# Performance work log

Measured on AMD Instinct MI355X. Metric: run time of the kernel, lower is better.

Reference implementation:

```python
import jax, jax.numpy as jnp
import numpy as np

B, M, N, T = 8192, 4, 8, 512  # groups, measurements, states, timesteps


def setup_inputs() -> dict:
    key = jax.random.key(0)
    k0, k1, k2, k3, k4, k5 = jax.random.split(key, 6)
    x = jax.random.normal(k0, (B, M, T), dtype=jnp.float32)
    # stable transition matrix (spectral radius < 1)
    F = (0.9 * jnp.eye(N) + 0.05 * jax.random.normal(k1, (N, N)) / np.sqrt(N)).astype(jnp.float32)
    H = (jax.random.normal(k2, (M, N)) / np.sqrt(N)).astype(jnp.float32)
    qa = jax.random.normal(k3, (N, N))
    Q = (0.05 * (qa @ qa.T) / N + 0.01 * jnp.eye(N)).astype(jnp.float32)
    ra = jax.random.normal(k4, (M, M))
    R = (0.1 * (ra @ ra.T) / M + 0.05 * jnp.eye(M)).astype(jnp.float32)
    initial_std_dev = (1.0 + jax.random.uniform(k5, (N,))).astype(jnp.float32)
    return {"x": x, "F": F, "H": H, "Q": Q, "R": R, "initial_std_dev": initial_std_dev}


def _kf_forward(x, F, H, Q, R, initial_std_dev):
    b, m, t = x.shape
    n = F.shape[0]
    dt = x.dtype
    # default_initializer: mean = 0 (len(initial_state)==num_states path with zeros),
    # cov = quad_form_diag(std, eye) = diag(std^2)
    mean0 = jnp.zeros((b, n, 1), dt)
    cov0 = jnp.broadcast_to(jnp.diag(initial_std_dev ** 2).astype(dt), (b, n, n))
    I_n = jnp.eye(n, dtype=dt)

    def step(carry, obs_t):  # obs_t: [b, m]
        mu, P = carry  # [b,n,1], [b,n,n]
        # --- predict ---
        mu = jnp.einsum('ij,bjk->bik', F, mu)
        P = jnp.einsum('ij,bjk,lk->bil', F, P, F) + Q
        out = jnp.einsum('mj,bjo->bmo', H, mu)[..., 0]  # [b, m]
        # --- update (no NaNs in obs -> update all slices) ---
        resid = obs_t[..., None] - out[..., None]  # [b,m,1]
        HP = jnp.einsum('mj,bjk->bmk', H, P)  # [b,m,n]
        S = jnp.einsum('bmj,nj->bmn', HP, H) + R  # [b,m,m]
        Sinv = jnp.linalg.inv(S)
        PHt = jnp.swapaxes(HP, 1, 2)  # P symmetric => P H^T = (H P)^T, [b,n,m]
        K = jnp.einsum('bnm,bmo->bno', PHt, Sinv)  # [b,n,m]
        mu_new = mu + jnp.einsum('bnm,bmo->bno', K, resid)
        # Joseph-stabilized covariance update
        ImKH = I_n - jnp.einsum('bnm,mj->bnj', K, H)  # [b,n,n]
        P_new = (jnp.einsum('bij,bjk,blk->bil', ImKH, P, ImKH)
                 + jnp.einsum('bim,mo,bko->bik', K, R, K))
        return (mu_new, P_new), out

    xs = jnp.moveaxis(x, 2, 0)  # [t, b, m]
    _, outs = jax.lax.scan(step, (mean0, cov0), xs)
    return jnp.moveaxis(outs, 0, 2)  # [b, m, t]


def reference(x, F, H, Q, R, initial_std_dev):
    return _kf_forward(x, F, H, Q, R, initial_std_dev)
```

## Files before the change

### kernel.cpp

```cpp
#include <hip/hip_runtime.h>


#define B_BATCH 8192
#define M_MEAS 4
#define N_ST 8
#define T_STEPS 512
#define CHUNK 16
#define NCHUNK (T_STEPS / CHUNK)

__device__ __forceinline__ void kf_producer(
    const float* __restrict__ Fp, const float* __restrict__ Hp,
    const float* __restrict__ Qp, const float* __restrict__ Rp,
    const float* __restrict__ stdp, float* __restrict__ Kws, int* flag)
{
    const int lane = threadIdx.x;
    const int i = lane >> 3, j = lane & 7;
    __shared__ float Pm[64], T1m[64], Vm[32], PPm[64], Am[64], Bm[64], Km[32];

    float Fi[8], Fj[8], Hm[4][8], HFm[4][8], HFr[8], QHi[4];
    float R2[4][4], Rr[4][4];
#pragma unroll
    for (int k = 0; k < 8; ++k) { Fi[k] = Fp[8 * i + k]; Fj[k] = Fp[8 * j + k]; }
#pragma unroll
    for (int m = 0; m < 4; ++m)
#pragma unroll
        for (int k = 0; k < 8; ++k) Hm[m][k] = Hp[8 * m + k];
#pragma unroll
    for (int m = 0; m < 4; ++m)
#pragma unroll
        for (int c = 0; c < 8; ++c) {
            float a = 0.f;
#pragma unroll
            for (int k = 0; k < 8; ++k) a += Hm[m][k] * Fp[8 * k + c];
            HFm[m][c] = a;
        }
#pragma unroll
    for (int c = 0; c < 8; ++c) {
        float a = 0.f;
#pragma unroll
        for (int k = 0; k < 8; ++k) a += Hp[8 * (i & 3) + k] * Fp[8 * k + c];
        HFr[c] = a;
    }
    const float Qij = Qp[lane];
#pragma unroll
    for (int m = 0; m < 4; ++m) {
        float a = 0.f;
#pragma unroll
        for (int k = 0; k < 8; ++k) a += Qp[8 * i + k] * Hm[m][k];
        QHi[m] = a;
    }
    {
        float HQ[4][8];
#pragma unroll
        for (int m = 0; m < 4; ++m)
#pragma unroll
            for (int c = 0; c < 8; ++c) {
                float a = 0.f;
#pragma unroll
                for (int l = 0; l < 8; ++l) a += Hm[m][l] * Qp[8 * l + c];
                HQ[m][c] = a;
            }
#pragma unroll
        for (int m = 0; m < 4; ++m)
#pragma unroll
            for (int n = 0; n < 4; ++n) {
                float a = Rp[4 * m + n];
#pragma unroll
                for (int k = 0; k < 8; ++k) a += HQ[m][k] * Hm[n][k];
                R2[m][n] = a;
                Rr[m][n] = Rp[4 * m + n];
            }
    }
    float pold;
    { float s0 = stdp[i]; pold = (i == j) ? s0 * s0 : 0.f; Pm[lane] = pold; }
    __syncthreads();

    int convcnt = 0;
    for (int t = 0; t < T_STEPS; ++t) {
        float4 pa = *(const float4*)&Pm[8 * j];
        float4 pb = *(const float4*)&Pm[8 * j + 4];
        float Pc[8] = {pa.x, pa.y, pa.z, pa.w, pb.x, pb.y, pb.z, pb.w};
        float t1 = 0.f, uo = 0.f;
#pragma unroll
        for (int k = 0; k < 8; ++k) { t1 += Fi[k] * Pc[k]; uo += HFr[k] * Pc[k]; }
        T1m[lane] = t1;
        if (i < 4) Vm[8 * i + j] = uo;
        __syncthreads();

        float4 ta = *(const float4*)&T1m[8 * i];
        float4 tb = *(const float4*)&T1m[8 * i + 4];
        float T1r[8] = {ta.x, ta.y, ta.z, ta.w, tb.x, tb.y, tb.z, tb.w};
        float pp = Qij;
#pragma unroll
        for (int k = 0; k < 8; ++k) pp += T1r[k] * Fj[k];
        float PPH[4];
#pragma unroll
        for (int m = 0; m < 4; ++m) {
            float a = QHi[m];
#pragma unroll
            for (int k = 0; k < 8; ++k) a += T1r[k] * HFm[m][k];
            PPH[m] = a;
        }
        PPm[lane] = pp;

        float Vr[4][8];
#pragma unroll
        for (int m = 0; m < 4; ++m) {
            float4 va = *(const float4*)&Vm[8 * m];
            float4 vb = *(const float4*)&Vm[8 * m + 4];
            Vr[m][0] = va.x; Vr[m][1] = va.y; Vr[m][2] = va.z; Vr[m][3] = va.w;
            Vr[m][4] = vb.x; Vr[m][5] = vb.y; Vr[m][6] = vb.z; Vr[m][7] = vb.w;
        }
        float S[4][4];
#pragma unroll
        for (int m = 0; m < 4; ++m)
#pragma unroll
            for (int n = m; n < 4; ++n) {
                float a = R2[m][n];
#pragma unroll
                for (int k = 0; k < 8; ++k) a += Vr[m][k] * HFm[n][k];
                S[m][n] = a; S[n][m] = a;
            }
        float SI[16];
        {
            const float A0 = S[0][0], A1 = S[0][1], A2 = S[0][2], A3 = S[0][3];
            const float A4 = S[1][0], A5 = S[1][1], A6 = S[1][2], A7 = S[1][3];
            const float A8 = S[2][0], A9 = S[2][1], A10 = S[2][2], A11 = S[2][3];
            const float A12 = S[3][0], A13 = S[3][1], A14 = S[3][2], A15 = S[3][3];
            float b00 = A0 * A5 - A1 * A4, b01 = A0 * A6 - A2 * A4;
            float b02 = A0 * A7 - A3 * A4, b03 = A1 * A6 - A2 * A5;
            float b04 = A1 * A7 - A3 * A5, b05 = A2 * A7 - A3 * A6;
            float b06 = A8 * A13 - A9 * A12, b07 = A8 * A14 - A10 * A12;
            float b08 = A8 * A15 - A11 * A12, b09 = A9 * A14 - A10 * A13;
            float b10 = A9 * A15 - A11 * A13, b11 = A10 * A15 - A11 * A14;
            float det = b00 * b11 - b01 * b10 + b02 * b09 + b03 * b08 -
                        b04 * b07 + b05 * b06;
            float rd = 1.0f / det;
            SI[0]  = ( A5 * b11 - A6 * b10 + A7 * b09) * rd;
            SI[1]  = (-A1 * b11 + A2 * b10 - A3 * b09) * rd;
            SI[2]  = ( A13 * b05 - A14 * b04 + A15 * b03) * rd;
            SI[3]  = (-A9 * b05 + A10 * b04 - A11 * b03) * rd;
            SI[4]  = (-A4 * b11 + A6 * b08 - A7 * b07) * rd;
            SI[5]  = ( A0 * b11 - A2 * b08 + A3 * b07) * rd;
            SI[6]  = (-A12 * b05 + A14 * b02 - A15 * b01) * rd;
            SI[7]  = ( A8 * b05 - A10 * b02 + A11 * b01) * rd;
            SI[8]  = ( A4 * b10 - A5 * b08 + A7 * b06) * rd;
            SI[9]  = (-A0 * b10 + A1 * b08 - A3 * b06) * rd;
            SI[10] = ( A12 * b04 - A13 * b02 + A15 * b00) * rd;
            SI[11] = (-A8 * b04 + A9 * b02 - A11 * b00) * rd;
            SI[12] = (-A4 * b09 + A5 * b07 - A6 * b06) * rd;
            SI[13] = ( A0 * b09 - A1 * b07 + A2 * b06) * rd;
            SI[14] = (-A12 * b03 + A13 * b01 - A14 * b00) * rd;
            SI[15] = ( A8 * b03 - A9 * b01 + A10 * b00) * rd;
        }
        float Kl[4];
#pragma unroll
        for (int m = 0; m < 4; ++m) {
            float a = 0.f;
#pragma unroll
            for (int p = 0; p < 4; ++p) a += PPH[p] * SI[4 * p + m];
            Kl[m] = a;
        }
        float Ar[8];
#pragma unroll
        for (int c = 0; c < 8; ++c) {
            float a = (i == c) ? 1.f : 0.f;
#pragma unroll
            for (int m = 0; m < 4; ++m) a -= Kl[m] * Hm[m][c];
            Ar[c] = a;
        }
        float Ei[4];
#pragma unroll
        for (int o = 0; o < 4; ++o) {
            float a = 0.f;
#pragma unroll
            for (int m = 0; m < 4; ++m) a += Kl[m] * Rr[m][o];
            Ei[o] = a;
        }
        const float aij = (j == 0) ? Ar[0] : (j == 1) ? Ar[1]
                        : (j == 2) ? Ar[2] : (j == 3) ? Ar[3]
                        : (j == 4) ? Ar[4] : (j == 5) ? Ar[5]
                        : (j == 6) ? Ar[6] : Ar[7];
        Am[lane] = aij;
        const float kj4 = (j == 0) ? Kl[0] : (j == 1) ? Kl[1]
                        : (j == 2) ? Kl[2] : Kl[3];
        if (j < 4) {
            Km[4 * i + j] = kj4;
            Kws[t * 32 + i * 4 + j] = kj4;
        }
        __syncthreads();

        float4 qa = *(const float4*)&PPm[8 * j];
        float4 qb = *(const float4*)&PPm[8 * j + 4];
        float PPc[8] = {qa.x, qa.y, qa.z, qa.w, qb.x, qb.y, qb.z, qb.w};
        float bv = 0.f;
#pragma unroll
        for (int k = 0; k < 8; ++k) bv += Ar[k] * PPc[k];
        Bm[lane] = bv;
        float4 aja = *(const float4*)&Am[8 * j];
        float4 ajb = *(const float4*)&Am[8 * j + 4];
        float Arj[8] = {aja.x, aja.y, aja.z, aja.w, ajb.x, ajb.y, ajb.z, ajb.w};
        float4 kjv = *(const float4*)&Km[4 * j];
        float Kj[4] = {kjv.x, kjv.y, kjv.z, kjv.w};
        __syncthreads();

        float4 ba = *(const float4*)&Bm[8 * i];
        float4 bb = *(const float4*)&Bm[8 * i + 4];
        float Br[8] = {ba.x, ba.y, ba.z, ba.w, bb.x, bb.y, bb.z, bb.w};
        float acc = 0.f;
#pragma unroll
        for (int k = 0; k < 8; ++k) acc += Br[k] * Arj[k];
#pragma unroll
        for (int o = 0; o < 4; ++o) acc += Ei[o] * Kj[o];
        Pm[lane] = acc;

        const float dp = fabsf(acc - pold);
        pold = acc;
        convcnt = __all(dp <= 1.5e-6f) ? convcnt + 1 : 0;
        if (convcnt >= 2 && t >= 31 && t < T_STEPS - 1) {
            if (j < 4) {
                for (int tt = t + 1; tt < T_STEPS; ++tt)
                    Kws[tt * 32 + i * 4 + j] = kj4;
            }
            if (flag != nullptr && lane == 0) {
                __hip_atomic_store(flag + 1, t, __ATOMIC_RELAXED,
                                   __HIP_MEMORY_SCOPE_AGENT);
                __threadfence();
                __hip_atomic_store(flag, NCHUNK, __ATOMIC_RELEASE,
                                   __HIP_MEMORY_SCOPE_AGENT);
            }
            break;
        }

        if (flag != nullptr && ((t & (CHUNK - 1)) == (CHUNK - 1))) {
            if (lane == 0) {
                __threadfence();
                __hip_atomic_store(flag, (t + 1) / CHUNK, __ATOMIC_RELEASE,
                                   __HIP_MEMORY_SCOPE_AGENT);
            }
        }
        __syncthreads();
    }
}

__device__ __forceinline__ void kf_consumer(
    const float* __restrict__ xp, const float* __restrict__ Fp,
    const float* __restrict__ Hp, const float* __restrict__ Kws,
    float* __restrict__ outp, int bblk, int* flag)
{
    const int b = bblk * 64 + threadIdx.x;

    float Fv[N_ST][N_ST];
#pragma unroll
    for (int n = 0; n < N_ST; ++n)
#pragma unroll
        for (int k = 0; k < N_ST; ++k) Fv[n][k] = Fp[8 * n + k];

    float G[M_MEAS][N_ST];
#pragma unroll
    for (int m = 0; m < M_MEAS; ++m) {
#pragma unroll
        for (int n = 0; n < N_ST; ++n) {
            float acc = 0.f;
#pragma unroll
            for (int k = 0; k < N_ST; ++k) acc += Hp[8 * m + k] * Fv[k][n];
            G[m][n] = acc;
        }
    }

    float mu[N_ST];
#pragma unroll
    for (int n = 0; n < N_ST; ++n) mu[n] = 0.f;

    const float* xb = xp + (size_t)b * (M_MEAS * T_STEPS);
    float* ob = outp + (size_t)b * (M_MEAS * T_STEPS);

    int lastseen = 0, tcf = 0;
    int g = 0;
    for (; g < 32; ++g) {
        if (flag != nullptr) {
            const int need = g + 1;
            if (lastseen < need) {
                while ((lastseen = __hip_atomic_load(
                            flag, __ATOMIC_RELAXED,
                            __HIP_MEMORY_SCOPE_AGENT)) < need)
                    __builtin_amdgcn_s_sleep(16);
                __builtin_amdgcn_fence(__ATOMIC_ACQUIRE, "agent");
            }
            if (tcf == 0)
                tcf = __hip_atomic_load(flag + 1, __ATOMIC_RELAXED,
                                        __HIP_MEMORY_SCOPE_AGENT);
            if (tcf > 0 && g * 16 >= tcf) break;
        }

        float ob16[M_MEAS][16];
#pragma unroll
        for (int u = 0; u < 4; ++u) {
            const int t4 = g * 4 + u;
            float4 xq[M_MEAS];
#pragma unroll
            for (int m = 0; m < M_MEAS; ++m)
                xq[m] = *(const float4*)(xb + m * T_STEPS + t4 * 4);

#pragma unroll
            for (int s = 0; s < 4; ++s) {
                const int t = t4 * 4 + s;
                const float4* kq = (const float4*)(Kws + t * 32);
                float4 kv[N_ST];
#pragma unroll
                for (int n = 0; n < N_ST; ++n) kv[n] = kq[n];

                float resid[M_MEAS];
#pragma unroll
                for (int m = 0; m < M_MEAS; ++m) {
                    float acc = 0.f;
#pragma unroll
                    for (int n = 0; n < N_ST; ++n) acc += G[m][n] * mu[n];
                    ob16[m][u * 4 + s] = acc;
                    const float xv = (s == 0) ? xq[m].x
                                   : (s == 1) ? xq[m].y
                                   : (s == 2) ? xq[m].z : xq[m].w;
                    resid[m] = xv - acc;
                }
                float nmu[N_ST];
#pragma unroll
                for (int n = 0; n < N_ST; ++n) {
                    float acc = 0.f;
#pragma unroll
                    for (int k = 0; k < N_ST; ++k) acc += Fv[n][k] * mu[k];
                    acc += kv[n].x * resid[0] + kv[n].y * resid[1] +
                           kv[n].z * resid[2] + kv[n].w * resid[3];
                    nmu[n] = acc;
                }
#pragma unroll
                for (int n = 0; n < N_ST; ++n) mu[n] = nmu[n];
            }
        }
#pragma unroll
        for (int m = 0; m < M_MEAS; ++m)
#pragma unroll
            for (int q = 0; q < 4; ++q)
                *(float4*)(ob + m * T_STEPS + g * 16 + q * 4) =
                    make_float4(ob16[m][4 * q], ob16[m][4 * q + 1],
                                ob16[m][4 * q + 2], ob16[m][4 * q + 3]);
    }

    if (g < 32) {
        float4 kvF[N_ST];
        {
            const float4* kqF = (const float4*)(Kws + (size_t)(g * 16) * 32);
#pragma unroll
            for (int n = 0; n < N_ST; ++n) kvF[n] = kqF[n];
        }
        for (; g < 32; ++g) {
            float ob16[M_MEAS][16];
#pragma unroll
            for (int u = 0; u < 4; ++u) {
                const int t4 = g * 4 + u;
                float4 xq[M_MEAS];
#pragma unroll
                for (int m = 0; m < M_MEAS; ++m)
                    xq[m] = *(const float4*)(xb + m * T_STEPS + t4 * 4);

#pragma unroll
                for (int s = 0; s < 4; ++s) {
                    float resid[M_MEAS];
#pragma unroll
                    for (int m = 0; m < M_MEAS; ++m) {
                        float acc = 0.f;
#pragma unroll
                        for (int n = 0; n < N_ST; ++n) acc += G[m][n] * mu[n];
                        ob16[m][u * 4 + s] = acc;
                        const float xv = (s == 0) ? xq[m].x
                                       : (s == 1) ? xq[m].y
                                       : (s == 2) ? xq[m].z : xq[m].w;
                        resid[m] = xv - acc;
                    }
                    float nmu[N_ST];
#pragma unroll
                    for (int n = 0; n < N_ST; ++n) {
                        float acc = 0.f;
#pragma unroll
                        for (int k = 0; k < N_ST; ++k) acc += Fv[n][k] * mu[k];
                        acc += kvF[n].x * resid[0] + kvF[n].y * resid[1] +
                               kvF[n].z * resid[2] + kvF[n].w * resid[3];
                        nmu[n] = acc;
                    }
#pragma unroll
                    for (int n = 0; n < N_ST; ++n) mu[n] = nmu[n];
                }
            }
#pragma unroll
            for (int m = 0; m < M_MEAS; ++m)
#pragma unroll
                for (int q = 0; q < 4; ++q)
                    *(float4*)(ob + m * T_STEPS + g * 16 + q * 4) =
                        make_float4(ob16[m][4 * q], ob16[m][4 * q + 1],
                                    ob16[m][4 * q + 2], ob16[m][4 * q + 3]);
        }
    }
}

__global__ __launch_bounds__(64) void kf_kernel(
    const float* __restrict__ x, const float* __restrict__ F,
    const float* __restrict__ H, const float* __restrict__ Q,
    const float* __restrict__ R, const float* __restrict__ std0,
    float* __restrict__ Kws, int* flag, float* __restrict__ out, int role)
{
    if (role == 0) {
        if (blockIdx.x == 0) kf_producer(F, H, Q, R, std0, Kws, flag);
        else kf_consumer(x, F, H, Kws, out, (int)blockIdx.x - 1, flag);
    } else if (role == 1) {
        kf_producer(F, H, Q, R, std0, Kws, nullptr);
    } else {
        kf_consumer(x, F, H, Kws, out, (int)blockIdx.x, nullptr);
    }
}

extern "C" void kernel_launch(void* const* d_in, const int* in_sizes, int n_in,
                              void* d_out, int out_size, void* d_ws, size_t ws_size,
                              hipStream_t stream) {
    const float* x   = (const float*)d_in[0];
    const float* F   = (const float*)d_in[1];
    const float* H   = (const float*)d_in[2];
    const float* Q   = (const float*)d_in[3];
    const float* R   = (const float*)d_in[4];
    const float* s0  = (const float*)d_in[5];
    float* out = (float*)d_out;
    float* Kws = (float*)d_ws;
    const size_t KWS_BYTES = (size_t)T_STEPS * 32 * sizeof(float);

    if (ws_size >= KWS_BYTES + 256) {
        int* flag = (int*)((char*)d_ws + KWS_BYTES);
        hipMemsetAsync(flag, 0, 2 * sizeof(int), stream);
        kf_kernel<<<dim3(1 + B_BATCH / 64), dim3(64), 0, stream>>>(
            x, F, H, Q, R, s0, Kws, flag, out, 0);
    } else {
        kf_kernel<<<dim3(1), dim3(64), 0, stream>>>(
            x, F, H, Q, R, s0, Kws, (int*)nullptr, out, 1);
        kf_kernel<<<dim3(B_BATCH / 64), dim3(64), 0, stream>>>(
            x, F, H, Q, R, s0, Kws, (int*)nullptr, out, 2);
    }
}
```

Before: 355.9 us.

## Replace producer LDS exchanges with cross-lane permutes; prefetch observations in consumer tail

The single-wave producer that runs the covariance recursion no longer exchanges P, T1, V, PP, A, K and B through shared memory with barriers. It now moves values between lanes with ds_bpermute and computes S = H·PP·Hᵀ through ds_swizzle butterfly reductions, which removes every __syncthreads from the serial 512-step loop. The consumer's tail loop is flattened to one iteration per 4 steps and loads observations two iterations ahead to hide global-load latency. The flattened loop indexes ob16 with a runtime value, which may push that array into scratch memory.

```diff
diff --git a/kernel.cpp b/kernel.cpp
--- a/kernel.cpp
+++ b/kernel.cpp
@@ -7,6 +7,14 @@
 #define T_STEPS 512
 #define CHUNK 16
 #define NCHUNK (T_STEPS / CHUNK)
+
+__device__ __forceinline__ float bperm_f(int byte_addr, float v) {
+    return __int_as_float(
+        __builtin_amdgcn_ds_bpermute(byte_addr, __float_as_int(v)));
+}
+#define SWZ_ADD(p, imm)                                                     \
+    p += __int_as_float(                                                    \
+        __builtin_amdgcn_ds_swizzle(__float_as_int(p), imm))
 
 __device__ __forceinline__ void kf_producer(
     const float* __restrict__ Fp, const float* __restrict__ Hp,
@@ -15,9 +23,15 @@
 {
     const int lane = threadIdx.x;
     const int i = lane >> 3, j = lane & 7;
-    __shared__ float Pm[64], T1m[64], Vm[32], PPm[64], Am[64], Bm[64], Km[32];
-
-    float Fi[8], Fj[8], Hm[4][8], HFm[4][8], HFr[8], QHi[4];
+
+    int A1[8], A2[8];
+#pragma unroll
+    for (int k = 0; k < 8; ++k) {
+        A1[k] = (8 * j + k) * 4;
+        A2[k] = (8 * i + k) * 4;
+    }
+
+    float Fi[8], Fj[8], Hm[4][8], HFm[4][8], HFr[8], QHi[4], HFcol[4];
     float R2[4][4], Rr[4][4];
 #pragma unroll
     for (int k = 0; k < 8; ++k) { Fi[k] = Fp[8 * i + k]; Fj[k] = Fp[8 * j + k]; }
@@ -40,6 +54,18 @@
 #pragma unroll
         for (int k = 0; k < 8; ++k) a += Hp[8 * (i & 3) + k] * Fp[8 * k + c];
         HFr[c] = a;
+    }
+    {
+        float Fcol[8];
+#pragma unroll
+        for (int k = 0; k < 8; ++k) Fcol[k] = Fp[8 * k + j];
+#pragma unroll
+        for (int n = 0; n < 4; ++n) {
+            float a = 0.f;
+#pragma unroll
+            for (int k = 0; k < 8; ++k) a += Hm[n][k] * Fcol[k];
+            HFcol[n] = a;
+        }
     }
     const float Qij = Qp[lane];
 #pragma unroll
@@ -71,28 +97,29 @@
                 Rr[m][n] = Rp[4 * m + n];
             }
     }
-    float pold;
-    { float s0 = stdp[i]; pold = (i == j) ? s0 * s0 : 0.f; Pm[lane] = pold; }
-    __syncthreads();
+
+    float pv, pold;
+    { float s0 = stdp[i]; pv = (i == j) ? s0 * s0 : 0.f; pold = pv; }
 
     int convcnt = 0;
     for (int t = 0; t < T_STEPS; ++t) {
-        float4 pa = *(const float4*)&Pm[8 * j];
-        float4 pb = *(const float4*)&Pm[8 * j + 4];
-        float Pc[8] = {pa.x, pa.y, pa.z, pa.w, pb.x, pb.y, pb.z, pb.w};
+        float Pc[8];
+#pragma unroll
+        for (int k = 0; k < 8; ++k) Pc[k] = bperm_f(A1[k], pv);
         float t1 = 0.f, uo = 0.f;
 #pragma unroll
         for (int k = 0; k < 8; ++k) { t1 += Fi[k] * Pc[k]; uo += HFr[k] * Pc[k]; }
-        T1m[lane] = t1;
-        if (i < 4) Vm[8 * i + j] = uo;
-        __syncthreads();
-
-        float4 ta = *(const float4*)&T1m[8 * i];
-        float4 tb = *(const float4*)&T1m[8 * i + 4];
-        float T1r[8] = {ta.x, ta.y, ta.z, ta.w, tb.x, tb.y, tb.z, tb.w};
+
+        float T1r[8];
+#pragma unroll
+        for (int k = 0; k < 8; ++k) T1r[k] = bperm_f(A2[k], t1);
         float pp = Qij;
 #pragma unroll
         for (int k = 0; k < 8; ++k) pp += T1r[k] * Fj[k];
+        float PPc[8];
+#pragma unroll
+        for (int k = 0; k < 8; ++k) PPc[k] = bperm_f(A1[k], pp);
+
         float PPH[4];
 #pragma unroll
         for (int m = 0; m < 4; ++m) {
@@ -101,35 +128,33 @@
             for (int k = 0; k < 8; ++k) a += T1r[k] * HFm[m][k];
             PPH[m] = a;
         }
-        PPm[lane] = pp;
-
-        float Vr[4][8];
+
+        float p0 = uo * HFcol[0], p1 = uo * HFcol[1];
+        float p2 = uo * HFcol[2], p3 = uo * HFcol[3];
+        SWZ_ADD(p0, 0x041F); SWZ_ADD(p1, 0x041F);
+        SWZ_ADD(p2, 0x041F); SWZ_ADD(p3, 0x041F);
+        SWZ_ADD(p0, 0x081F); SWZ_ADD(p1, 0x081F);
+        SWZ_ADD(p2, 0x081F); SWZ_ADD(p3, 0x081F);
+        SWZ_ADD(p0, 0x101F); SWZ_ADD(p1, 0x101F);
+        SWZ_ADD(p2, 0x101F); SWZ_ADD(p3, 0x101F);
+        float S[4][4];
 #pragma unroll
         for (int m = 0; m < 4; ++m) {
-            float4 va = *(const float4*)&Vm[8 * m];
-            float4 vb = *(const float4*)&Vm[8 * m + 4];
-            Vr[m][0] = va.x; Vr[m][1] = va.y; Vr[m][2] = va.z; Vr[m][3] = va.w;
-            Vr[m][4] = vb.x; Vr[m][5] = vb.y; Vr[m][6] = vb.z; Vr[m][7] = vb.w;
-        }
-        float S[4][4];
-#pragma unroll
-        for (int m = 0; m < 4; ++m)
-#pragma unroll
-            for (int n = m; n < 4; ++n) {
-                float a = R2[m][n];
-#pragma unroll
-                for (int k = 0; k < 8; ++k) a += Vr[m][k] * HFm[n][k];
-                S[m][n] = a; S[n][m] = a;
-            }
+            S[m][0] = bperm_f(32 * m, p0) + R2[m][0];
+            S[m][1] = bperm_f(32 * m, p1) + R2[m][1];
+            S[m][2] = bperm_f(32 * m, p2) + R2[m][2];
+            S[m][3] = bperm_f(32 * m, p3) + R2[m][3];
+        }
+
         float SI[16];
         {
-            const float A0 = S[0][0], A1 = S[0][1], A2 = S[0][2], A3 = S[0][3];
+            const float A0 = S[0][0], A1_ = S[0][1], A2_ = S[0][2], A3 = S[0][3];
             const float A4 = S[1][0], A5 = S[1][1], A6 = S[1][2], A7 = S[1][3];
             const float A8 = S[2][0], A9 = S[2][1], A10 = S[2][2], A11 = S[2][3];
             const float A12 = S[3][0], A13 = S[3][1], A14 = S[3][2], A15 = S[3][3];
-            float b00 = A0 * A5 - A1 * A4, b01 = A0 * A6 - A2 * A4;
-            float b02 = A0 * A7 - A3 * A4, b03 = A1 * A6 - A2 * A5;
-            float b04 = A1 * A7 - A3 * A5, b05 = A2 * A7 - A3 * A6;
+            float b00 = A0 * A5 - A1_ * A4, b01 = A0 * A6 - A2_ * A4;
+            float b02 = A0 * A7 - A3 * A4, b03 = A1_ * A6 - A2_ * A5;
+            float b04 = A1_ * A7 - A3 * A5, b05 = A2_ * A7 - A3 * A6;
             float b06 = A8 * A13 - A9 * A12, b07 = A8 * A14 - A10 * A12;
             float b08 = A8 * A15 - A11 * A12, b09 = A9 * A14 - A10 * A13;
             float b10 = A9 * A15 - A11 * A13, b11 = A10 * A15 - A11 * A14;
@@ -137,19 +162,19 @@
                         b04 * b07 + b05 * b06;
             float rd = 1.0f / det;
             SI[0]  = ( A5 * b11 - A6 * b10 + A7 * b09) * rd;
-            SI[1]  = (-A1 * b11 + A2 * b10 - A3 * b09) * rd;
+            SI[1]  = (-A1_ * b11 + A2_ * b10 - A3 * b09) * rd;
             SI[2]  = ( A13 * b05 - A14 * b04 + A15 * b03) * rd;
             SI[3]  = (-A9 * b05 + A10 * b04 - A11 * b03) * rd;
             SI[4]  = (-A4 * b11 + A6 * b08 - A7 * b07) * rd;
-            SI[5]  = ( A0 * b11 - A2 * b08 + A3 * b07) * rd;
+            SI[5]  = ( A0 * b11 - A2_ * b08 + A3 * b07) * rd;
             SI[6]  = (-A12 * b05 + A14 * b02 - A15 * b01) * rd;
             SI[7]  = ( A8 * b05 - A10 * b02 + A11 * b01) * rd;
             SI[8]  = ( A4 * b10 - A5 * b08 + A7 * b06) * rd;
-            SI[9]  = (-A0 * b10 + A1 * b08 - A3 * b06) * rd;
+            SI[9]  = (-A0 * b10 + A1_ * b08 - A3 * b06) * rd;
             SI[10] = ( A12 * b04 - A13 * b02 + A15 * b00) * rd;
             SI[11] = (-A8 * b04 + A9 * b02 - A11 * b00) * rd;
             SI[12] = (-A4 * b09 + A5 * b07 - A6 * b06) * rd;
-            SI[13] = ( A0 * b09 - A1 * b07 + A2 * b06) * rd;
+            SI[13] = ( A0 * b09 - A1_ * b07 + A2_ * b06) * rd;
             SI[14] = (-A12 * b03 + A13 * b01 - A14 * b00) * rd;
             SI[15] = ( A8 * b03 - A9 * b01 + A10 * b00) * rd;
         }
@@ -181,38 +206,29 @@
                         : (j == 2) ? Ar[2] : (j == 3) ? Ar[3]
                         : (j == 4) ? Ar[4] : (j == 5) ? Ar[5]
                         : (j == 6) ? Ar[6] : Ar[7];
-        Am[lane] = aij;
         const float kj4 = (j == 0) ? Kl[0] : (j == 1) ? Kl[1]
                         : (j == 2) ? Kl[2] : Kl[3];
-        if (j < 4) {
-            Km[4 * i + j] = kj4;
-            Kws[t * 32 + i * 4 + j] = kj4;
-        }
-        __syncthreads();
-
-        float4 qa = *(const float4*)&PPm[8 * j];
-        float4 qb = *(const float4*)&PPm[8 * j + 4];
-        float PPc[8] = {qa.x, qa.y, qa.z, qa.w, qb.x, qb.y, qb.z, qb.w};
+        if (j < 4) Kws[t * 32 + i * 4 + j] = kj4;
+
+        float Arj[8];
+#pragma unroll
+        for (int k = 0; k < 8; ++k) Arj[k] = bperm_f(A1[k], aij);
+        float Kj[4];
+#pragma unroll
+        for (int o = 0; o < 4; ++o) Kj[o] = bperm_f(A1[o], kj4);
+
         float bv = 0.f;
 #pragma unroll
         for (int k = 0; k < 8; ++k) bv += Ar[k] * PPc[k];
-        Bm[lane] = bv;
-        float4 aja = *(const float4*)&Am[8 * j];
-        float4 ajb = *(const float4*)&Am[8 * j + 4];
-        float Arj[8] = {aja.x, aja.y, aja.z, aja.w, ajb.x, ajb.y, ajb.z, ajb.w};
-        float4 kjv = *(const float4*)&Km[4 * j];
-        float Kj[4] = {kjv.x, kjv.y, kjv.z, kjv.w};
-        __syncthreads();
-
-        float4 ba = *(const float4*)&Bm[8 * i];
-        float4 bb = *(const float4*)&Bm[8 * i + 4];
-        float Br[8] = {ba.x, ba.y, ba.z, ba.w, bb.x, bb.y, bb.z, bb.w};
+        float Br[8];
+#pragma unroll
+        for (int k = 0; k < 8; ++k) Br[k] = bperm_f(A2[k], bv);
         float acc = 0.f;
 #pragma unroll
         for (int k = 0; k < 8; ++k) acc += Br[k] * Arj[k];
 #pragma unroll
         for (int o = 0; o < 4; ++o) acc += Ei[o] * Kj[o];
-        Pm[lane] = acc;
+        pv = acc;
 
         const float dp = fabsf(acc - pold);
         pold = acc;
@@ -239,7 +255,6 @@
                                    __HIP_MEMORY_SCOPE_AGENT);
             }
         }
-        __syncthreads();
     }
 }
 
@@ -352,51 +367,64 @@
 #pragma unroll
             for (int n = 0; n < N_ST; ++n) kvF[n] = kqF[n];
         }
-        for (; g < 32; ++g) {
-            float ob16[M_MEAS][16];
-#pragma unroll
-            for (int u = 0; u < 4; ++u) {
-                const int t4 = g * 4 + u;
-                float4 xq[M_MEAS];
+        int t4 = g * 4;
+        float4 xq[M_MEAS], xn1[M_MEAS];
+#pragma unroll
+        for (int m = 0; m < M_MEAS; ++m)
+            xq[m] = *(const float4*)(xb + m * T_STEPS + t4 * 4);
+        if (t4 + 1 < 128) {
+#pragma unroll
+            for (int m = 0; m < M_MEAS; ++m)
+                xn1[m] = *(const float4*)(xb + m * T_STEPS + (t4 + 1) * 4);
+        }
+        float ob16[M_MEAS][16];
+        for (; t4 < 128; ++t4) {
+            float4 xn2[M_MEAS] = {xn1[0], xn1[1], xn1[2], xn1[3]};
+            if (t4 + 2 < 128) {
 #pragma unroll
                 for (int m = 0; m < M_MEAS; ++m)
-                    xq[m] = *(const float4*)(xb + m * T_STEPS + t4 * 4);
-
-#pragma unroll
-                for (int s = 0; s < 4; ++s) {
-                    float resid[M_MEAS];
-#pragma unroll
-                    for (int m = 0; m < M_MEAS; ++m) {
-                        float acc = 0.f;
-#pragma unroll
-                        for (int n = 0; n < N_ST; ++n) acc += G[m][n] * mu[n];
-                        ob16[m][u * 4 + s] = acc;
-                        const float xv = (s == 0) ? xq[m].x
-                                       : (s == 1) ? xq[m].y
-                                       : (s == 2) ? xq[m].z : xq[m].w;
-                        resid[m] = xv - acc;
-                    }
-                    float nmu[N_ST];
-#pragma unroll
-                    for (int n = 0; n < N_ST; ++n) {
-                        float acc = 0.f;
-#pragma unroll
-                        for (int k = 0; k < N_ST; ++k) acc += Fv[n][k] * mu[k];
-                        acc += kvF[n].x * resid[0] + kvF[n].y * resid[1] +
-                               kvF[n].z * resid[2] + kvF[n].w * resid[3];
-                        nmu[n] = acc;
-                    }
-#pragma unroll
-                    for (int n = 0; n < N_ST; ++n) mu[n] = nmu[n];
+                    xn2[m] = *(const float4*)(xb + m * T_STEPS + (t4 + 2) * 4);
+            }
+            const int u = t4 & 3;
+#pragma unroll
+            for (int s = 0; s < 4; ++s) {
+                float resid[M_MEAS];
+#pragma unroll
+                for (int m = 0; m < M_MEAS; ++m) {
+                    float acc = 0.f;
+#pragma unroll
+                    for (int n = 0; n < N_ST; ++n) acc += G[m][n] * mu[n];
+                    ob16[m][u * 4 + s] = acc;
+                    const float xv = (s == 0) ? xq[m].x
+                                   : (s == 1) ? xq[m].y
+                                   : (s == 2) ? xq[m].z : xq[m].w;
+                    resid[m] = xv - acc;
                 }
-            }
-#pragma unroll
-            for (int m = 0; m < M_MEAS; ++m)
-#pragma unroll
-                for (int q = 0; q < 4; ++q)
-                    *(float4*)(ob + m * T_STEPS + g * 16 + q * 4) =
-                        make_float4(ob16[m][4 * q], ob16[m][4 * q + 1],
-                                    ob16[m][4 * q + 2], ob16[m][4 * q + 3]);
+                float nmu[N_ST];
+#pragma unroll
+                for (int n = 0; n < N_ST; ++n) {
+                    float acc = 0.f;
+#pragma unroll
+                    for (int k = 0; k < N_ST; ++k) acc += Fv[n][k] * mu[k];
+                    acc += kvF[n].x * resid[0] + kvF[n].y * resid[1] +
+                           kvF[n].z * resid[2] + kvF[n].w * resid[3];
+                    nmu[n] = acc;
+                }
+#pragma unroll
+                for (int n = 0; n < N_ST; ++n) mu[n] = nmu[n];
+            }
+            if (u == 3) {
+                const int gg = t4 >> 2;
+#pragma unroll
+                for (int m = 0; m < M_MEAS; ++m)
+#pragma unroll
+                    for (int q = 0; q < 4; ++q)
+                        *(float4*)(ob + m * T_STEPS + gg * 16 + q * 4) =
+                            make_float4(ob16[m][4 * q], ob16[m][4 * q + 1],
+                                        ob16[m][4 * q + 2], ob16[m][4 * q + 3]);
+            }
+#pragma unroll
+            for (int m = 0; m < M_MEAS; ++m) { xq[m] = xn1[m]; xn1[m] = xn2[m]; }
         }
     }
 }
```

After: 507.2 us. 42.5% more time.
